# Kernel optimization log

Measured on AMD Instinct MI355X. Metric: run time of the kernel, lower is better.

## Reference

```python
import jax, jax.numpy as jnp
import numpy as np

N_NODES = 100000
N_EDGES = 1600000
D_IN = 128
D_OUT = 128


def setup_inputs() -> dict:
    key = jax.random.key(0)
    k1, k2, k3 = jax.random.split(key, 3)
    x = jax.random.normal(k1, (N_NODES, D_IN), dtype=jnp.float32)
    edge_index = jax.random.randint(k2, (2, N_EDGES), 0, N_NODES, dtype=jnp.int64)
    # Glorot-style init for the GCN weight, zero bias (PyG defaults)
    W = jax.random.normal(k3, (D_IN, D_OUT), dtype=jnp.float32) * (1.0 / np.sqrt(D_IN))
    b = jnp.zeros((D_OUT,), dtype=jnp.float32)
    return {"x": x, "edge_index": edge_index, "W": W, "b": b}


def reference(x, edge_index, W, b):
    # GCNConv (PyG defaults: add_self_loops=True, normalize=True):
    #   out = D^{-1/2} (A + I) D^{-1/2} (X W) + b
    # Dropout is identity in eval mode.
    n = x.shape[0]
    loop = jnp.arange(n, dtype=edge_index.dtype)
    src = jnp.concatenate([edge_index[0], loop])  # [E + N]
    dst = jnp.concatenate([edge_index[1], loop])  # [E + N]

    h = x @ W  # [N, D_OUT] -- transform before aggregation (fewer FLOPs if D_OUT <= D_IN)

    # Degree of each node counting self-loops, computed over targets.
    ones = jnp.ones(dst.shape[0], dtype=h.dtype)
    deg = jax.ops.segment_sum(ones, dst, num_segments=n)  # [N]
    deg_inv_sqrt = jnp.where(deg > 0, jax.lax.rsqrt(deg), 0.0)

    # Symmetric normalization per edge: d_src^{-1/2} * d_dst^{-1/2}
    norm = deg_inv_sqrt[src] * deg_inv_sqrt[dst]  # [E + N]

    # Gather messages, scale, scatter-add to targets.
    msgs = h[src] * norm[:, None]  # [E + N, D_OUT]
    out = jax.ops.segment_sum(msgs, dst, num_segments=n)  # [N, D_OUT]
    return out + b
```

## Files before the change

### kernel.cpp

```cpp
#include <hip/hip_runtime.h>

#define DD 128
#define CAP 12288

typedef __attribute__((ext_vector_type(8))) short bf16x8;
typedef __attribute__((ext_vector_type(4))) float f32x4;

__device__ inline unsigned short f2b(float f) {
    unsigned int u = __float_as_uint(f);
    u += 0x7fffu + ((u >> 16) & 1u);
    return (unsigned short)(u >> 16);
}

__device__ inline void bacc16f(float4& a, float4& b, uint4 v, float s) {
    a.x += __uint_as_float(v.x << 16) * s;
    a.y += __uint_as_float(v.x & 0xffff0000u) * s;
    a.z += __uint_as_float(v.y << 16) * s;
    a.w += __uint_as_float(v.y & 0xffff0000u) * s;
    b.x += __uint_as_float(v.z << 16) * s;
    b.y += __uint_as_float(v.z & 0xffff0000u) * s;
    b.z += __uint_as_float(v.w << 16) * s;
    b.w += __uint_as_float(v.w & 0xffff0000u) * s;
}

__global__ __launch_bounds__(256) void k_pre(const float* __restrict__ W,
                                             unsigned short* __restrict__ Wt,
                                             int* __restrict__ cur, int nbuck) {
    int bid = blockIdx.x;
    if (bid < 64) {
        int idx = bid * 256 + threadIdx.x;
        int k = idx >> 7, c = idx & 127;
        Wt[c * DD + k] = f2b(W[k * DD + c]);
    } else {
        int b = (bid - 64) * 256 + threadIdx.x;
        if (b < nbuck) cur[b] = b * CAP;
    }
}

__global__ __launch_bounds__(256) void k_binA(const int* __restrict__ src,
                                              const int* __restrict__ dst, int E,
                                              int chunk, int nbuck,
                                              int* __restrict__ cur,
                                              int* __restrict__ binned) {
    __shared__ int hist[256];
    __shared__ int base[256];
    __shared__ int curs[256];
    const int t = threadIdx.x;
    const int e0 = blockIdx.x * chunk;
    const int e1 = min(e0 + chunk, E);

    if (t < 256) { hist[t] = 0; curs[t] = 0; }
    __syncthreads();
    for (int e = e0 + t; e < e1; e += 256)
        atomicAdd(&hist[dst[e] >> 9], 1);
    __syncthreads();
    if (t < nbuck && hist[t] > 0)
        base[t] = atomicAdd(&cur[t], hist[t]);
    __syncthreads();
    for (int e = e0 + t; e < e1; e += 256) {
        int d = dst[e];
        int b = d >> 9;
        int p = atomicAdd(&curs[b], 1);
        int idx = base[b] + p;
        if (idx < (b + 1) * CAP)
            binned[idx] = (src[e] << 9) | (d & 511);
    }
}

__global__ __launch_bounds__(512) void k_fuse(int* __restrict__ binned,
                                              const int* __restrict__ cur,
                                              int* __restrict__ off,
                                              int* __restrict__ cnt,
                                              float* __restrict__ dinv,
                                              const float* __restrict__ x,
                                              const unsigned short* __restrict__ Wt,
                                              unsigned short* __restrict__ hs,
                                              int n, int nbuck) {
    __shared__ int hist[512];
    __shared__ int curs[512];
    __shared__ int sorted[CAP];
    const int t = threadIdx.x;

    if (blockIdx.x < (unsigned)nbuck) {
        const int b = blockIdx.x;
        const int base = b * CAP;
        const int cb = cur[b] - base;

        hist[t] = 0;
        __syncthreads();
        for (int i = t; i < cb; i += 512)
            atomicAdd(&hist[binned[base + i] & 511], 1);
        __syncthreads();
        int v = hist[t];
        for (int st = 1; st < 512; st <<= 1) {
            int tv = (t >= st) ? hist[t - st] : 0;
            __syncthreads();
            hist[t] += tv;
            __syncthreads();
        }
        int excl = hist[t] - v;
        curs[t] = excl;
        int d = b * 512 + t;
        if (d < n) {
            off[d]  = base + excl;
            cnt[d]  = v;
            dinv[d] = rsqrtf((float)v + 1.0f);
        }
        __syncthreads();
        for (int i = t; i < cb; i += 512) {
            int pk = binned[base + i];
            int p = atomicAdd(&curs[pk & 511], 1);
            sorted[p] = pk >> 9;
        }
        __syncthreads();
        for (int i = t; i < cb; i += 512)
            binned[base + i] = sorted[i];
    } else {
        const int gb = blockIdx.x - nbuck;
        const int wave = t >> 6, lane = t & 63;
        const int rowbase = gb * 256 + wave * 32;
        const int l15 = lane & 15, l4 = lane >> 4;

        bf16x8 a[2][4];
        #pragma unroll
        for (int rb = 0; rb < 2; ++rb) {
            int r = rowbase + rb * 16 + l15;
            int rc = min(r, n - 1);
            const float* xr = x + (size_t)rc * DD;
            #pragma unroll
            for (int kc = 0; kc < 4; ++kc) {
                int k0 = kc * 32 + l4 * 8;
                float4 f0 = *(const float4*)(xr + k0);
                float4 f1 = *(const float4*)(xr + k0 + 4);
                bf16x8 fr;
                fr[0] = (short)f2b(f0.x); fr[1] = (short)f2b(f0.y);
                fr[2] = (short)f2b(f0.z); fr[3] = (short)f2b(f0.w);
                fr[4] = (short)f2b(f1.x); fr[5] = (short)f2b(f1.y);
                fr[6] = (short)f2b(f1.z); fr[7] = (short)f2b(f1.w);
                a[rb][kc] = fr;
            }
        }

        #pragma unroll
        for (int cb8 = 0; cb8 < 8; ++cb8) {
            int c0 = cb8 * 16;
            f32x4 acc[2] = {};
            #pragma unroll
            for (int kc = 0; kc < 4; ++kc) {
                bf16x8 bfrag = *(const bf16x8*)(Wt + (size_t)(c0 + l15) * DD + kc * 32 + l4 * 8);
                #pragma unroll
                for (int rb = 0; rb < 2; ++rb)
                    acc[rb] = __builtin_amdgcn_mfma_f32_16x16x32_bf16(a[rb][kc], bfrag, acc[rb], 0, 0, 0);
            }
            #pragma unroll
            for (int rb = 0; rb < 2; ++rb) {
                int r0 = rowbase + rb * 16 + l4 * 4;
                #pragma unroll
                for (int vv = 0; vv < 4; ++vv) {
                    int r = r0 + vv;
                    if (r < n)
                        hs[(size_t)r * DD + c0 + l15] = f2b(acc[rb][vv]);
                }
            }
        }
    }
}

__global__ __launch_bounds__(256, 8) void k_agg(const uint4* __restrict__ hsr,
                                                const int* __restrict__ ssrc,
                                                const int* __restrict__ off,
                                                const int* __restrict__ cnt,
                                                const float* __restrict__ dinv,
                                                const float* __restrict__ bias,
                                                float* __restrict__ out, int n) {
    const int t = threadIdx.x;
    const int wave = t >> 6, lane = t & 63;
    const int q  = lane >> 4;
    const int ql = lane & 15;
    const int d = blockIdx.x * 4 + wave;
    if (d >= n) return;

    const int s0 = off[d];
    const int c  = cnt[d];
    const float di = dinv[d];

    float4 accA = {0.f, 0.f, 0.f, 0.f};
    float4 accB = {0.f, 0.f, 0.f, 0.f};

    uint4 vself = hsr[(size_t)d * 16 + ql];

    int idx[6];
    #pragma unroll
    for (int r = 0; r < 6; ++r) {
        int e = r * 4 + q;
        idx[r] = ssrc[s0 + ((e < c) ? e : 0)];
    }
    #pragma unroll
    for (int r = 0; r < 6; ++r) {
        int e = r * 4 + q;
        idx[r] = (e < c) ? idx[r] : d;
    }

    uint4 val[6];
    float sc[6];
    #pragma unroll
    for (int r = 0; r < 6; ++r) {
        val[r] = hsr[(size_t)idx[r] * 16 + ql];
        sc[r]  = dinv[idx[r]];
    }

    if (q == 0) bacc16f(accA, accB, vself, di);
    #pragma unroll
    for (int r = 0; r < 6; ++r) {
        int e = r * 4 + q;
        if (e < c) bacc16f(accA, accB, val[r], sc[r]);
    }

    for (int i = 24 + q; i < c; i += 4) {
        int s = ssrc[s0 + i];
        uint4 v = hsr[(size_t)s * 16 + ql];
        bacc16f(accA, accB, v, dinv[s]);
    }

    #pragma unroll
    for (int m = 16; m <= 32; m <<= 1) {
        accA.x += __shfl_xor(accA.x, m);
        accA.y += __shfl_xor(accA.y, m);
        accA.z += __shfl_xor(accA.z, m);
        accA.w += __shfl_xor(accA.w, m);
        accB.x += __shfl_xor(accB.x, m);
        accB.y += __shfl_xor(accB.y, m);
        accB.z += __shfl_xor(accB.z, m);
        accB.w += __shfl_xor(accB.w, m);
    }

    if (q == 0) {
        float4 b0 = ((const float4*)bias)[ql * 2];
        float4 b1 = ((const float4*)bias)[ql * 2 + 1];
        float4 o0, o1;
        o0.x = accA.x * di + b0.x;
        o0.y = accA.y * di + b0.y;
        o0.z = accA.z * di + b0.z;
        o0.w = accA.w * di + b0.w;
        o1.x = accB.x * di + b1.x;
        o1.y = accB.y * di + b1.y;
        o1.z = accB.z * di + b1.z;
        o1.w = accB.w * di + b1.w;
        float4* orow = (float4*)(out + (size_t)d * DD);
        orow[ql * 2]     = o0;
        orow[ql * 2 + 1] = o1;
    }
}

extern "C" void kernel_launch(void* const* d_in, const int* in_sizes, int n_in,
                              void* d_out, int out_size, void* d_ws, size_t ws_size,
                              hipStream_t stream) {
    const float* x  = (const float*)d_in[0];
    const int*   ei = (const int*)d_in[1];
    const float* W  = (const float*)d_in[2];
    const float* b  = (const float*)d_in[3];
    float* out = (float*)d_out;

    const int n = in_sizes[0] / DD;
    const int E = in_sizes[1] / 2;
    const int* src = ei;
    const int* dst = ei + E;

    const int nbuck = (n + 511) >> 9;

    unsigned short* hs = (unsigned short*)d_ws;
    unsigned short* Wt = hs + (size_t)n * DD;
    int*   binned = (int*)(Wt + DD * DD);
    int*   off    = binned + (size_t)nbuck * CAP;
    int*   cnt    = off + n;
    float* dinv   = (float*)(cnt + n);
    int*   cur    = (int*)(dinv + n);

    const int nblkA = 1024;
    const int chunk = (E + nblkA - 1) / nblkA;

    const int ngemm = (n + 255) / 256;

    k_pre <<<64 + (nbuck + 255) / 256, 256, 0, stream>>>(W, Wt, cur, nbuck);
    k_binA<<<nblkA, 256, 0, stream>>>(src, dst, E, chunk, nbuck, cur, binned);
    k_fuse<<<nbuck + ngemm, 512, 0, stream>>>(binned, cur, off, cnt, dinv,
                                              x, Wt, hs, n, nbuck);
    k_agg <<<(n + 3) / 4, 256, 0, stream>>>((const uint4*)hs, binned, off, cnt,
                                            dinv, b, out, n);
}
```

Measured before the change: 134.5 us.

## Split GEMM work across binning and sort kernels to overlap with edge bucketing

Moves roughly half of the X·W GEMM row blocks (195×256 rows) into the edge-binning kernel as extra blocks, using a 4×16-row tile per wave. The remaining rows stay with the per-bucket sort kernel, offset by growoff. The aim is to fill idle compute units during the atomic-heavy binning phase and shorten the tail of the sort+GEMM kernel. The trade-offs are a hardcoded split point that assumes n exceeds 195×256, and higher register pressure in the combined binning kernel.

```diff
diff --git a/kernel.cpp b/kernel.cpp
--- a/kernel.cpp
+++ b/kernel.cpp
@@ -37,45 +37,99 @@
     }
 }
 
-__global__ __launch_bounds__(256) void k_binA(const int* __restrict__ src,
-                                              const int* __restrict__ dst, int E,
-                                              int chunk, int nbuck,
-                                              int* __restrict__ cur,
-                                              int* __restrict__ binned) {
-    __shared__ int hist[256];
-    __shared__ int base[256];
-    __shared__ int curs[256];
+__global__ __launch_bounds__(256) void k_fA(const int* __restrict__ src,
+                                            const int* __restrict__ dst, int E,
+                                            int chunk, int nbuck,
+                                            int* __restrict__ cur,
+                                            int* __restrict__ binned,
+                                            const float* __restrict__ x,
+                                            const unsigned short* __restrict__ Wt,
+                                            unsigned short* __restrict__ hs,
+                                            int n, int nbinA) {
     const int t = threadIdx.x;
-    const int e0 = blockIdx.x * chunk;
-    const int e1 = min(e0 + chunk, E);
-
-    if (t < 256) { hist[t] = 0; curs[t] = 0; }
-    __syncthreads();
-    for (int e = e0 + t; e < e1; e += 256)
-        atomicAdd(&hist[dst[e] >> 9], 1);
-    __syncthreads();
-    if (t < nbuck && hist[t] > 0)
-        base[t] = atomicAdd(&cur[t], hist[t]);
-    __syncthreads();
-    for (int e = e0 + t; e < e1; e += 256) {
-        int d = dst[e];
-        int b = d >> 9;
-        int p = atomicAdd(&curs[b], 1);
-        int idx = base[b] + p;
-        if (idx < (b + 1) * CAP)
-            binned[idx] = (src[e] << 9) | (d & 511);
-    }
-}
-
-__global__ __launch_bounds__(512) void k_fuse(int* __restrict__ binned,
-                                              const int* __restrict__ cur,
-                                              int* __restrict__ off,
-                                              int* __restrict__ cnt,
-                                              float* __restrict__ dinv,
-                                              const float* __restrict__ x,
-                                              const unsigned short* __restrict__ Wt,
-                                              unsigned short* __restrict__ hs,
-                                              int n, int nbuck) {
+    if ((int)blockIdx.x < nbinA) {
+        __shared__ int hist[256];
+        __shared__ int base[256];
+        __shared__ int curs[256];
+        const int e0 = blockIdx.x * chunk;
+        const int e1 = min(e0 + chunk, E);
+
+        if (t < 256) { hist[t] = 0; curs[t] = 0; }
+        __syncthreads();
+        for (int e = e0 + t; e < e1; e += 256)
+            atomicAdd(&hist[dst[e] >> 9], 1);
+        __syncthreads();
+        if (t < nbuck && hist[t] > 0)
+            base[t] = atomicAdd(&cur[t], hist[t]);
+        __syncthreads();
+        for (int e = e0 + t; e < e1; e += 256) {
+            int d = dst[e];
+            int b = d >> 9;
+            int p = atomicAdd(&curs[b], 1);
+            int idx = base[b] + p;
+            if (idx < (b + 1) * CAP)
+                binned[idx] = (src[e] << 9) | (d & 511);
+        }
+        return;
+    }
+
+    const int wave = t >> 6, lane = t & 63;
+    const int rowbase = (blockIdx.x - nbinA) * 256 + wave * 64;
+    const int l15 = lane & 15, l4 = lane >> 4;
+
+    bf16x8 a[4][4];
+    #pragma unroll
+    for (int rb = 0; rb < 4; ++rb) {
+        int r = rowbase + rb * 16 + l15;
+        int rc = min(r, n - 1);
+        const float* xr = x + (size_t)rc * DD;
+        #pragma unroll
+        for (int kc = 0; kc < 4; ++kc) {
+            int k0 = kc * 32 + l4 * 8;
+            float4 f0 = *(const float4*)(xr + k0);
+            float4 f1 = *(const float4*)(xr + k0 + 4);
+            bf16x8 fr;
+            fr[0] = (short)f2b(f0.x); fr[1] = (short)f2b(f0.y);
+            fr[2] = (short)f2b(f0.z); fr[3] = (short)f2b(f0.w);
+            fr[4] = (short)f2b(f1.x); fr[5] = (short)f2b(f1.y);
+            fr[6] = (short)f2b(f1.z); fr[7] = (short)f2b(f1.w);
+            a[rb][kc] = fr;
+        }
+    }
+
+    #pragma unroll
+    for (int cb = 0; cb < 8; ++cb) {
+        int c0 = cb * 16;
+        f32x4 acc[4] = {};
+        #pragma unroll
+        for (int kc = 0; kc < 4; ++kc) {
+            bf16x8 bfrag = *(const bf16x8*)(Wt + (size_t)(c0 + l15) * DD + kc * 32 + l4 * 8);
+            #pragma unroll
+            for (int rb = 0; rb < 4; ++rb)
+                acc[rb] = __builtin_amdgcn_mfma_f32_16x16x32_bf16(a[rb][kc], bfrag, acc[rb], 0, 0, 0);
+        }
+        #pragma unroll
+        for (int rb = 0; rb < 4; ++rb) {
+            int r0 = rowbase + rb * 16 + l4 * 4;
+            #pragma unroll
+            for (int vv = 0; vv < 4; ++vv) {
+                int r = r0 + vv;
+                if (r < n)
+                    hs[(size_t)r * DD + c0 + l15] = f2b(acc[rb][vv]);
+            }
+        }
+    }
+}
+
+__global__ __launch_bounds__(512) void k_fB(int* __restrict__ binned,
+                                            const int* __restrict__ cur,
+                                            int* __restrict__ off,
+                                            int* __restrict__ cnt,
+                                            float* __restrict__ dinv,
+                                            const float* __restrict__ x,
+                                            const unsigned short* __restrict__ Wt,
+                                            unsigned short* __restrict__ hs,
+                                            int n, int nbuck, int growoff) {
     __shared__ int hist[512];
     __shared__ int curs[512];
     __shared__ int sorted[CAP];
@@ -115,52 +169,53 @@
         __syncthreads();
         for (int i = t; i < cb; i += 512)
             binned[base + i] = sorted[i];
-    } else {
-        const int gb = blockIdx.x - nbuck;
-        const int wave = t >> 6, lane = t & 63;
-        const int rowbase = gb * 256 + wave * 32;
-        const int l15 = lane & 15, l4 = lane >> 4;
-
-        bf16x8 a[2][4];
+        return;
+    }
+
+    const int gb = blockIdx.x - nbuck;
+    const int wave = t >> 6, lane = t & 63;
+    const int rowbase = growoff + gb * 256 + wave * 32;
+    const int l15 = lane & 15, l4 = lane >> 4;
+
+    bf16x8 a[2][4];
+    #pragma unroll
+    for (int rb = 0; rb < 2; ++rb) {
+        int r = rowbase + rb * 16 + l15;
+        int rc = min(r, n - 1);
+        const float* xr = x + (size_t)rc * DD;
+        #pragma unroll
+        for (int kc = 0; kc < 4; ++kc) {
+            int k0 = kc * 32 + l4 * 8;
+            float4 f0 = *(const float4*)(xr + k0);
+            float4 f1 = *(const float4*)(xr + k0 + 4);
+            bf16x8 fr;
+            fr[0] = (short)f2b(f0.x); fr[1] = (short)f2b(f0.y);
+            fr[2] = (short)f2b(f0.z); fr[3] = (short)f2b(f0.w);
+            fr[4] = (short)f2b(f1.x); fr[5] = (short)f2b(f1.y);
+            fr[6] = (short)f2b(f1.z); fr[7] = (short)f2b(f1.w);
+            a[rb][kc] = fr;
+        }
+    }
+
+    #pragma unroll
+    for (int cb8 = 0; cb8 < 8; ++cb8) {
+        int c0 = cb8 * 16;
+        f32x4 acc[2] = {};
+        #pragma unroll
+        for (int kc = 0; kc < 4; ++kc) {
+            bf16x8 bfrag = *(const bf16x8*)(Wt + (size_t)(c0 + l15) * DD + kc * 32 + l4 * 8);
+            #pragma unroll
+            for (int rb = 0; rb < 2; ++rb)
+                acc[rb] = __builtin_amdgcn_mfma_f32_16x16x32_bf16(a[rb][kc], bfrag, acc[rb], 0, 0, 0);
+        }
         #pragma unroll
         for (int rb = 0; rb < 2; ++rb) {
-            int r = rowbase + rb * 16 + l15;
-            int rc = min(r, n - 1);
-            const float* xr = x + (size_t)rc * DD;
+            int r0 = rowbase + rb * 16 + l4 * 4;
             #pragma unroll
-            for (int kc = 0; kc < 4; ++kc) {
-                int k0 = kc * 32 + l4 * 8;
-                float4 f0 = *(const float4*)(xr + k0);
-                float4 f1 = *(const float4*)(xr + k0 + 4);
-                bf16x8 fr;
-                fr[0] = (short)f2b(f0.x); fr[1] = (short)f2b(f0.y);
-                fr[2] = (short)f2b(f0.z); fr[3] = (short)f2b(f0.w);
-                fr[4] = (short)f2b(f1.x); fr[5] = (short)f2b(f1.y);
-                fr[6] = (short)f2b(f1.z); fr[7] = (short)f2b(f1.w);
-                a[rb][kc] = fr;
-            }
-        }
-
-        #pragma unroll
-        for (int cb8 = 0; cb8 < 8; ++cb8) {
-            int c0 = cb8 * 16;
-            f32x4 acc[2] = {};
-            #pragma unroll
-            for (int kc = 0; kc < 4; ++kc) {
-                bf16x8 bfrag = *(const bf16x8*)(Wt + (size_t)(c0 + l15) * DD + kc * 32 + l4 * 8);
-                #pragma unroll
-                for (int rb = 0; rb < 2; ++rb)
-                    acc[rb] = __builtin_amdgcn_mfma_f32_16x16x32_bf16(a[rb][kc], bfrag, acc[rb], 0, 0, 0);
-            }
-            #pragma unroll
-            for (int rb = 0; rb < 2; ++rb) {
-                int r0 = rowbase + rb * 16 + l4 * 4;
-                #pragma unroll
-                for (int vv = 0; vv < 4; ++vv) {
-                    int r = r0 + vv;
-                    if (r < n)
-                        hs[(size_t)r * DD + c0 + l15] = f2b(acc[rb][vv]);
-                }
+            for (int vv = 0; vv < 4; ++vv) {
+                int r = r0 + vv;
+                if (r < n)
+                    hs[(size_t)r * DD + c0 + l15] = f2b(acc[rb][vv]);
             }
         }
     }
@@ -279,12 +334,15 @@
     const int nblkA = 1024;
     const int chunk = (E + nblkA - 1) / nblkA;
 
-    const int ngemm = (n + 255) / 256;
-
-    k_pre <<<64 + (nbuck + 255) / 256, 256, 0, stream>>>(W, Wt, cur, nbuck);
-    k_binA<<<nblkA, 256, 0, stream>>>(src, dst, E, chunk, nbuck, cur, binned);
-    k_fuse<<<nbuck + ngemm, 512, 0, stream>>>(binned, cur, off, cnt, dinv,
-                                              x, Wt, hs, n, nbuck);
-    k_agg <<<(n + 3) / 4, 256, 0, stream>>>((const uint4*)hs, binned, off, cnt,
-                                            dinv, b, out, n);
-}
+    const int ngA = 195;
+    const int growoff = ngA * 256;
+    const int ngB = (n - growoff + 255) / 256;
+
+    k_pre<<<64 + (nbuck + 255) / 256, 256, 0, stream>>>(W, Wt, cur, nbuck);
+    k_fA <<<nblkA + ngA, 256, 0, stream>>>(src, dst, E, chunk, nbuck, cur, binned,
+                                           x, Wt, hs, n, nblkA);
+    k_fB <<<nbuck + ngB, 512, 0, stream>>>(binned, cur, off, cnt, dinv,
+                                           x, Wt, hs, n, nbuck, growoff);
+    k_agg<<<(n + 3) / 4, 256, 0, stream>>>((const uint4*)hs, binned, off, cnt,
+                                           dinv, b, out, n);
+}
```

New measurement: 134.3 us. About the same (-0.2%).
